# Optimization experiments

Measured on AMD Instinct MI355X. Metric: run time of the kernel, lower is better.

## Reference

```python
import jax, jax.numpy as jnp
import numpy as np

N_PTS = 1024
IMG_H, IMG_W = 128, 128
NSIGMA = 3.0
NEAR = 0.01
COV_BLUR = 0.3  # 3DGS-style screen-space dilation (pixels^2)


def setup_inputs() -> dict:
    key = jax.random.key(0)
    k1, k2, k3, k4 = jax.random.split(key, 4)
    coords = jax.random.uniform(k1, (N_PTS, 3), minval=-1.0, maxval=1.0, dtype=jnp.float32)
    A = jax.random.normal(k2, (N_PTS, 3, 3), dtype=jnp.float32) * 0.05
    covariances = jnp.einsum('nij,nkj->nik', A, A) + 1e-4 * jnp.eye(3, dtype=jnp.float32)
    colors = jax.random.uniform(k3, (N_PTS, 3), dtype=jnp.float32)
    alphas = jax.random.uniform(k4, (N_PTS,), minval=0.1, maxval=0.9, dtype=jnp.float32)
    # world-to-camera: identity rotation, camera 4 units back so all depths in [3,5]
    W = jnp.eye(4, dtype=jnp.float32).at[2, 3].set(4.0)
    K = jnp.array([[150.0, 0.0, 64.0], [0.0, 150.0, 64.0], [0.0, 0.0, 1.0]], dtype=jnp.float32)
    return {"coords": coords, "covariances": covariances, "colors": colors,
            "alphas": alphas, "W": W, "K": K}


def _rasterize(coords, covariances, colors, alphas, W, K):
    R, t = W[:3, :3], W[:3, 3]
    p_cam = coords @ R.T + t                      # [N,3] camera-space points
    tx, ty, tz = p_cam[:, 0], p_cam[:, 1], p_cam[:, 2]
    fx, fy, cx, cy = K[0, 0], K[1, 1], K[0, 2], K[1, 2]
    inv_z = 1.0 / jnp.maximum(tz, NEAR)
    u = fx * tx * inv_z + cx                      # [N] pixel x of splat center
    v = fy * ty * inv_z + cy                      # [N] pixel y
    # perspective Jacobian J: [N,2,3]
    zeros = jnp.zeros_like(tz)
    J = jnp.stack([
        jnp.stack([fx * inv_z, zeros, -fx * tx * inv_z ** 2], axis=-1),
        jnp.stack([zeros, fy * inv_z, -fy * ty * inv_z ** 2], axis=-1),
    ], axis=1)
    sig_cam = jnp.einsum('ij,njk,lk->nil', R, covariances, R)      # [N,3,3]
    sig2d = jnp.einsum('nij,njk,nlk->nil', J, sig_cam, J)          # [N,2,2]
    sig2d = sig2d + COV_BLUR * jnp.eye(2, dtype=sig2d.dtype)
    det = sig2d[:, 0, 0] * sig2d[:, 1, 1] - sig2d[:, 0, 1] ** 2
    inv_det = 1.0 / det
    ca = sig2d[:, 1, 1] * inv_det   # conic coefficients of Sigma2D^{-1}
    cc = sig2d[:, 0, 0] * inv_det
    cb = -sig2d[:, 0, 1] * inv_det
    valid = tz > NEAR
    # front-to-back depth sort
    order = jnp.argsort(tz)
    u, v = u[order], v[order]
    ca, cb, cc = ca[order], cb[order], cc[order]
    a_s = jnp.clip(alphas[order], 0.0, 1.0)
    col_s = colors[order]
    valid = valid[order]
    # pixel centers
    xs = jnp.arange(IMG_W, dtype=jnp.float32) + 0.5
    ys = jnp.arange(IMG_H, dtype=jnp.float32) + 0.5
    dx = xs[None, :] - u[:, None]                 # [N,W]
    dy = ys[None, :] - v[:, None]                 # [N,H]
    # squared Mahalanobis distance per gaussian per pixel: [N,H,W]
    q = (ca[:, None, None] * (dx ** 2)[:, None, :]
         + cc[:, None, None] * (dy ** 2)[:, :, None]
         + 2.0 * cb[:, None, None] * dy[:, :, None] * dx[:, None, :])
    g = jnp.exp(-0.5 * q)
    inside = (q <= NSIGMA ** 2) & valid[:, None, None]
    alpha_px = jnp.where(inside, a_s[:, None, None] * g, 0.0)
    alpha_px = jnp.minimum(alpha_px, 0.999)
    # exclusive transmittance along sorted gaussian axis
    T = jnp.cumprod(1.0 - alpha_px, axis=0)
    T_excl = jnp.concatenate([jnp.ones_like(T[:1]), T[:-1]], axis=0)
    w = alpha_px * T_excl                         # [N,H,W]
    img = jnp.einsum('nhw,nc->chw', w, col_s)     # [3,H,W]
    return img


def reference(coords, covariances, colors, alphas, W, K):
    return _rasterize(coords, covariances, colors, alphas, W, K)
```

## Files before the change

### kernel.cpp

```cpp
#include <hip/hip_runtime.h>

#define N_PTS   1024
#define IMG_H   128
#define IMG_W   128
#define NPIX    (IMG_H * IMG_W)
#define NEAR    0.01f
#define COV_BLUR 0.3f
#define NCHUNK  32
#define CHUNK_SZ (N_PTS / NCHUNK)
#define PT_STRIDE 12
#define PXS     4
#define ROWSTEP (NPIX / PXS)
#define CBLK    256
#define NSTRIP  (ROWSTEP / CBLK)

#define S_SCALE (-0.72134752044448170368f)
#define QLIM    (-6.49212768400033533312f)

__global__ __launch_bounds__(256) void k_sortpre(
    const float* __restrict__ coords,
    const float* __restrict__ covs,
    const float* __restrict__ colors,
    const float* __restrict__ alphas,
    const float* __restrict__ Wm,
    const float* __restrict__ Km,
    float* __restrict__ sorted)
{
    __shared__ __align__(16) float scoord[N_PTS * 3];
    __shared__ __align__(16) unsigned long long skey[N_PTS];
    int tid = threadIdx.x;

    {
        float4* sc4 = (float4*)scoord;
        const float4* g4 = (const float4*)coords;
        #pragma unroll
        for (int j = 0; j < 3; j++) sc4[tid + j * 256] = g4[tid + j * 256];
    }

    float R[3][3], tv[3];
    #pragma unroll
    for (int r = 0; r < 3; r++) {
        #pragma unroll
        for (int c = 0; c < 3; c++) R[r][c] = Wm[r * 4 + c];
        tv[r] = Wm[r * 4 + 3];
    }
    float fx = Km[0], fy = Km[4], cx = Km[2], cy = Km[5];

    __syncthreads();

    #pragma unroll
    for (int q = 0; q < 4; q++) {
        int j = tid + q * 256;
        float c0 = scoord[3 * j], c1 = scoord[3 * j + 1], c2 = scoord[3 * j + 2];
        float d = R[2][0] * c0 + R[2][1] * c1 + R[2][2] * c2 + tv[2];
        unsigned int b = __float_as_uint(d);
        b ^= ((unsigned int)((int)b >> 31)) | 0x80000000u;
        skey[j] = ((unsigned long long)b << 10) | (unsigned int)j;
    }
    __syncthreads();

    int i = blockIdx.x * 256 + tid;

    float S[3][3];
    #pragma unroll
    for (int r = 0; r < 3; r++)
        #pragma unroll
        for (int c = 0; c < 3; c++) S[r][c] = covs[i * 9 + r * 3 + c];
    float colR = colors[3 * i + 0];
    float colG = colors[3 * i + 1];
    float colB = colors[3 * i + 2];
    float aRaw = alphas[i];

    float c0 = scoord[3 * i], c1 = scoord[3 * i + 1], c2 = scoord[3 * i + 2];
    float tz = R[2][0] * c0 + R[2][1] * c1 + R[2][2] * c2 + tv[2];
    unsigned long long mykey = skey[i];

    int rank = 0;
    const ulonglong2* sk2 = (const ulonglong2*)skey;
    #pragma unroll 16
    for (int jj = 0; jj < N_PTS / 2; jj++) {
        ulonglong2 k2 = sk2[jj];
        rank += (k2.x < mykey);
        rank += (k2.y < mykey);
    }

    float tx = R[0][0] * c0 + R[0][1] * c1 + R[0][2] * c2 + tv[0];
    float ty = R[1][0] * c0 + R[1][1] * c1 + R[1][2] * c2 + tv[1];

    float invz = 1.0f / fmaxf(tz, NEAR);
    float u = fx * tx * invz + cx;
    float v = fy * ty * invz + cy;
    float J00 = fx * invz;
    float J02 = -fx * tx * invz * invz;
    float J11 = fy * invz;
    float J12 = -fy * ty * invz * invz;

    float M[3][3];
    #pragma unroll
    for (int r = 0; r < 3; r++)
        #pragma unroll
        for (int c = 0; c < 3; c++)
            M[r][c] = R[r][0] * S[0][c] + R[r][1] * S[1][c] + R[r][2] * S[2][c];
    float Sc[3][3];
    #pragma unroll
    for (int r = 0; r < 3; r++)
        #pragma unroll
        for (int c = 0; c < 3; c++)
            Sc[r][c] = M[r][0] * R[c][0] + M[r][1] * R[c][1] + M[r][2] * R[c][2];

    float js0_0 = J00 * Sc[0][0] + J02 * Sc[2][0];
    float js0_1 = J00 * Sc[0][1] + J02 * Sc[2][1];
    float js0_2 = J00 * Sc[0][2] + J02 * Sc[2][2];
    float js1_1 = J11 * Sc[1][1] + J12 * Sc[2][1];
    float js1_2 = J11 * Sc[1][2] + J12 * Sc[2][2];

    float s00 = J00 * js0_0 + J02 * js0_2 + COV_BLUR;
    float s01 = J11 * js0_1 + J12 * js0_2;
    float s11 = J11 * js1_1 + J12 * js1_2 + COV_BLUR;

    float det = s00 * s11 - s01 * s01;
    float invdet = 1.0f / det;
    float caS  = s11 * invdet * S_SCALE;
    float ccS  = s00 * invdet * S_SCALE;
    float cb2S = -2.0f * s01 * invdet * S_SCALE;

    float a = fminf(fmaxf(aRaw, 0.0f), 1.0f);
    if (!(tz > NEAR)) a = 0.0f;
    float l2a  = __log2f(a);
    float qlim = QLIM + l2a;

    float4* dst = (float4*)(sorted + rank * PT_STRIDE);
    dst[0] = make_float4(tz, u, v, caS);
    dst[1] = make_float4(cb2S, ccS, qlim, colR);
    dst[2] = make_float4(colG, colB, l2a, 0.0f);
}

__global__ __launch_bounds__(CBLK) void k_composite(
    const float* __restrict__ sorted, float* __restrict__ partials)
{
    int chunk = blockIdx.y;
    int pix = blockIdx.x * CBLK + threadIdx.x;

    __shared__ float4 sg[CHUNK_SZ * 3];
    const float4* src = (const float4*)sorted + chunk * CHUNK_SZ * 3;
    if (threadIdx.x < CHUNK_SZ * 3) sg[threadIdx.x] = src[threadIdx.x];
    __syncthreads();

    float px  = (float)(pix & (IMG_W - 1)) + 0.5f;
    float py0 = (float)(pix >> 7) + 0.5f;

    float T[PXS], cr[PXS], cg[PXS], cb[PXS];
    #pragma unroll
    for (int s = 0; s < PXS; s++) { T[s] = 1.0f; cr[s] = cg[s] = cb[s] = 0.0f; }

    #pragma unroll
    for (int k = 0; k < CHUNK_SZ; k++) {
        float4 A = sg[3 * k + 0];
        float4 B = sg[3 * k + 1];
        float4 C = sg[3 * k + 2];
        float dx    = px - A.y;
        float cadxx = fmaf(A.w * dx, dx, C.z);
        float cb2dx = B.x * dx;
        #pragma unroll
        for (int s = 0; s < PXS; s++) {
            float dy  = py0 + 32.0f * s - A.z;
            float inr = fmaf(B.y, dy, cb2dx);
            float qq  = fmaf(dy, inr, cadxx);
            float e   = exp2f(qq);
            float apx = (qq >= B.z) ? e : 0.0f;
            float w = T[s] * apx;
            cr[s] = fmaf(w, B.w, cr[s]);
            cg[s] = fmaf(w, C.x, cg[s]);
            cb[s] = fmaf(w, C.y, cb[s]);
            T[s]  = fmaf(-apx, T[s], T[s]);
        }
    }

    float4* p4 = (float4*)partials;
    #pragma unroll
    for (int s = 0; s < PXS; s++)
        p4[chunk * NPIX + pix + s * ROWSTEP] = make_float4(cr[s], cg[s], cb[s], T[s]);
}

__global__ __launch_bounds__(256) void k_combine(
    const float* __restrict__ partials, float* __restrict__ out)
{
    int I = blockIdx.x * 256 + threadIdx.x;
    float T = 1.0f, r = 0.0f, g = 0.0f, b = 0.0f;
    #pragma unroll
    for (int c = 0; c < NCHUNK; c++) {
        float4 p = ((const float4*)partials)[c * NPIX + I];
        r = fmaf(T, p.x, r);
        g = fmaf(T, p.y, g);
        b = fmaf(T, p.z, b);
        T *= p.w;
    }
    out[0 * NPIX + I] = r;
    out[1 * NPIX + I] = g;
    out[2 * NPIX + I] = b;
}

extern "C" void kernel_launch(void* const* d_in, const int* in_sizes, int n_in,
                              void* d_out, int out_size, void* d_ws, size_t ws_size,
                              hipStream_t stream)
{
    const float* coords = (const float*)d_in[0];
    const float* covs   = (const float*)d_in[1];
    const float* colors = (const float*)d_in[2];
    const float* alphas = (const float*)d_in[3];
    const float* Wm     = (const float*)d_in[4];
    const float* Km     = (const float*)d_in[5];

    float* ws = (float*)d_ws;
    float* sorted   = ws;
    float* partials = ws + N_PTS * PT_STRIDE;

    k_sortpre<<<dim3(N_PTS / 256), dim3(256), 0, stream>>>(
        coords, covs, colors, alphas, Wm, Km, sorted);
    k_composite<<<dim3(NSTRIP, NCHUNK), dim3(CBLK), 0, stream>>>(sorted, partials);
    k_combine<<<dim3(NPIX / 256), dim3(256), 0, stream>>>(partials, (float*)d_out);
}
```

Baseline: 99.61 us.

## Fuse combine pass into composite kernel via global atomic counter barrier

Removes the separate combine kernel launch. Every composite block bumps a global counter after writing its partials, and the first 64 blocks spin until all 512 blocks have finished, then each merges the chunk partials for 256 pixels. The goal is to save one launch and its gap between kernels. In exchange it depends on all blocks being co-resident or scheduled without deadlock, since the low-index blocks spin waiting on the others, and the counter is reset inside the sort kernel. launch_bounds gains a minimum of 2 blocks per unit.

```diff
diff --git a/kernel.cpp b/kernel.cpp
--- a/kernel.cpp
+++ b/kernel.cpp
@@ -13,6 +13,8 @@
 #define ROWSTEP (NPIX / PXS)
 #define CBLK    256
 #define NSTRIP  (ROWSTEP / CBLK)
+#define NBLK    (NSTRIP * NCHUNK)
+#define NCOMB   (NPIX / 256)
 
 #define S_SCALE (-0.72134752044448170368f)
 #define QLIM    (-6.49212768400033533312f)
@@ -24,11 +26,14 @@
     const float* __restrict__ alphas,
     const float* __restrict__ Wm,
     const float* __restrict__ Km,
-    float* __restrict__ sorted)
+    float* __restrict__ sorted,
+    unsigned int* __restrict__ ctr)
 {
     __shared__ __align__(16) float scoord[N_PTS * 3];
     __shared__ __align__(16) unsigned long long skey[N_PTS];
     int tid = threadIdx.x;
+
+    if (blockIdx.x == 0 && tid == 0) *ctr = 0u;
 
     {
         float4* sc4 = (float4*)scoord;
@@ -135,15 +140,19 @@
     dst[2] = make_float4(colG, colB, l2a, 0.0f);
 }
 
-__global__ __launch_bounds__(CBLK) void k_composite(
-    const float* __restrict__ sorted, float* __restrict__ partials)
+__global__ __launch_bounds__(CBLK, 2) void k_composite(
+    const float* __restrict__ sorted,
+    float* __restrict__ partials,
+    float* __restrict__ out,
+    unsigned int* __restrict__ ctr)
 {
     int chunk = blockIdx.y;
-    int pix = blockIdx.x * CBLK + threadIdx.x;
+    int tid = threadIdx.x;
+    int pix = blockIdx.x * CBLK + tid;
 
     __shared__ float4 sg[CHUNK_SZ * 3];
     const float4* src = (const float4*)sorted + chunk * CHUNK_SZ * 3;
-    if (threadIdx.x < CHUNK_SZ * 3) sg[threadIdx.x] = src[threadIdx.x];
+    if (tid < CHUNK_SZ * 3) sg[tid] = src[tid];
     __syncthreads();
 
     float px  = (float)(pix & (IMG_W - 1)) + 0.5f;
@@ -180,24 +189,34 @@
     #pragma unroll
     for (int s = 0; s < PXS; s++)
         p4[chunk * NPIX + pix + s * ROWSTEP] = make_float4(cr[s], cg[s], cb[s], T[s]);
-}
-
-__global__ __launch_bounds__(256) void k_combine(
-    const float* __restrict__ partials, float* __restrict__ out)
-{
-    int I = blockIdx.x * 256 + threadIdx.x;
-    float T = 1.0f, r = 0.0f, g = 0.0f, b = 0.0f;
-    #pragma unroll
-    for (int c = 0; c < NCHUNK; c++) {
-        float4 p = ((const float4*)partials)[c * NPIX + I];
-        r = fmaf(T, p.x, r);
-        g = fmaf(T, p.y, g);
-        b = fmaf(T, p.z, b);
-        T *= p.w;
-    }
-    out[0 * NPIX + I] = r;
-    out[1 * NPIX + I] = g;
-    out[2 * NPIX + I] = b;
+
+    __threadfence();
+    __syncthreads();
+    if (tid == 0) atomicAdd(ctr, 1u);
+
+    int lb = blockIdx.y * NSTRIP + blockIdx.x;
+    if (lb < NCOMB) {
+        if (tid == 0) {
+            while (__hip_atomic_load(ctr, __ATOMIC_ACQUIRE,
+                                     __HIP_MEMORY_SCOPE_AGENT) < (unsigned)NBLK)
+                __builtin_amdgcn_s_sleep(1);
+        }
+        __syncthreads();
+
+        int I = lb * 256 + tid;
+        float T2 = 1.0f, r = 0.0f, g = 0.0f, b = 0.0f;
+        #pragma unroll
+        for (int c = 0; c < NCHUNK; c++) {
+            float4 p = ((const float4*)partials)[c * NPIX + I];
+            r = fmaf(T2, p.x, r);
+            g = fmaf(T2, p.y, g);
+            b = fmaf(T2, p.z, b);
+            T2 *= p.w;
+        }
+        out[0 * NPIX + I] = r;
+        out[1 * NPIX + I] = g;
+        out[2 * NPIX + I] = b;
+    }
 }
 
 extern "C" void kernel_launch(void* const* d_in, const int* in_sizes, int n_in,
@@ -214,9 +233,10 @@
     float* ws = (float*)d_ws;
     float* sorted   = ws;
     float* partials = ws + N_PTS * PT_STRIDE;
+    unsigned int* ctr = (unsigned int*)(partials + NCHUNK * NPIX * 4);
 
     k_sortpre<<<dim3(N_PTS / 256), dim3(256), 0, stream>>>(
-        coords, covs, colors, alphas, Wm, Km, sorted);
-    k_composite<<<dim3(NSTRIP, NCHUNK), dim3(CBLK), 0, stream>>>(sorted, partials);
-    k_combine<<<dim3(NPIX / 256), dim3(256), 0, stream>>>(partials, (float*)d_out);
+        coords, covs, colors, alphas, Wm, Km, sorted, ctr);
+    k_composite<<<dim3(NSTRIP, NCHUNK), dim3(CBLK), 0, stream>>>(
+        sorted, partials, (float*)d_out, ctr);
 }
```

New measurement: 151.5 us. +52.1%, slower.
